# Kernel optimization log

Measured on AMD Instinct MI355X. Metric: run time of the kernel, lower is better.

The kernel has to match this reference:

```python
import jax, jax.numpy as jnp
import numpy as np

BALL_BBOX_SIZE = 40.0
PLAYER_DS = 16
BALL_DS = 4
MAX_DET = 100
B, HP, WP = 64, 68, 120
HB, WB = 272, 480


def _nms2d(x):
    # keep only local maxima in a 3x3 window (kornia-style NonMaximaSuppression2d)
    m = jax.lax.reduce_window(x, -jnp.inf, jax.lax.max, (1, 1, 3, 3), (1, 1, 1, 1), 'SAME')
    return jnp.where(x == m, x, jnp.zeros((), x.dtype))


def _detect_from_map(conf_logits, ds, max_det, bbox_map):
    # conf_logits: [B,2,h,w]; bbox_map: [B,4,h,w] or None
    p = jax.nn.softmax(conf_logits, axis=1)          # softmax applied in forward() for 'detect' phase
    conf = _nms2d(p)[:, 1]                           # [B,h,w], positive-class channel
    bsz, h, w = conf.shape
    flat = conf.reshape(bsz, h * w)
    values, indices = jax.lax.top_k(flat, max_det)   # == full descending sort truncated to max_det
    fds = jnp.float32(ds)
    xc = (indices % w).astype(jnp.float32) * fds + (fds - 1.0) / 2.0
    yc = (indices // w).astype(jnp.float32) * fds + (fds - 1.0) / 2.0
    if bbox_map is None:
        # ball: fixed-size boxes, zero center offsets
        temp = jnp.zeros((bsz, 4, max_det), jnp.float32).at[:, 2:4].set(BALL_BBOX_SIZE)
    else:
        # offsets/sizes are fractions of image size -> scale to pixels, then gather per top-k cell
        scale = jnp.array([w * ds, h * ds, w * ds, h * ds], jnp.float32).reshape(1, 4, 1)
        bm = bbox_map.reshape(bsz, 4, h * w) * scale
        temp = jnp.take_along_axis(bm, indices[:, None, :], axis=2)  # [B,4,max_det]
    bx = xc + temp[:, 0]
    by = yc + temp[:, 1]
    return jnp.stack([bx - 0.5 * temp[:, 2],
                      by - 0.5 * temp[:, 3],
                      bx + 0.5 * temp[:, 2],
                      by + 0.5 * temp[:, 3],
                      values], axis=-1)              # [B,max_det,5] = x1,y1,x2,y2,score


def setup_inputs() -> dict:
    key = jax.random.key(0)
    k1, k2, k3 = jax.random.split(key, 3)
    return {
        'player_feature_map': jax.random.normal(k1, (B, 2, HP, WP), jnp.float32),
        'player_bbox': jax.random.normal(k2, (B, 4, HP, WP), jnp.float32) * 0.05,
        'ball_feature_map': jax.random.normal(k3, (B, 2, HB, WB), jnp.float32),
    }


def reference(player_feature_map, player_bbox, ball_feature_map):
    player_det = _detect_from_map(player_feature_map, PLAYER_DS, MAX_DET, player_bbox)
    ball_det = _detect_from_map(ball_feature_map, BALL_DS, MAX_DET, None)
    return (player_det, ball_det)
```

## Files before the change

kernel.cpp:

```cpp
#include <hip/hip_runtime.h>
#include <stdint.h>
#include <math.h>

#define TPB   512
#define KTOP  100
#define K1    128
#define KSLOT 192
#define CAP   768
#define SR    8

#define HB 272
#define WB 480
#define NSB 34
#define HP 68
#define WP 120
#define NSP 9
#define NB 64

__device__ __forceinline__ float G_exact(float D) {
    float t = -fabsf(D);
    float etf = (float)exp((double)t);
    return (D > 0.0f) ? __fdiv_rn(1.0f, __fadd_rn(etf, 1.0f))
                      : __fdiv_rn(etf, __fadd_rn(1.0f, etf));
}

__device__ __forceinline__ uint32_t flip_f32(float D) {
    uint32_t u = __float_as_uint(D);
    return (u & 0x80000000u) ? ~u : (u | 0x80000000u);
}

__device__ __forceinline__ int agg_push(int* ctr, bool active) {
    uint64_t m = __ballot(active);
    int pos = -1;
    if (active) {
        int lane = threadIdx.x & 63;
        int lead = __ffsll((unsigned long long)m) - 1;
        int before = (int)__popcll(m & ((1ull << lane) - 1ull));
        int base = 0;
        if (lane == lead) base = atomicAdd(ctr, (int)__popcll(m));
        base = __shfl(base, lead, 64);
        pos = base + before;
    }
    return pos;
}

__device__ __forceinline__ void hist_clustered(uint32_t* hist, uint32_t bin, bool active) {
    uint64_t todo = __ballot(active);
    while (todo) {
        int lead = __ffsll((unsigned long long)todo) - 1;
        uint32_t b = (uint32_t)__shfl((int)bin, lead, 64);
        uint64_t same = __ballot(active && (bin == b));
        if ((int)(threadIdx.x & 63) == lead) atomicAdd(&hist[b], (uint32_t)__popcll(same));
        todo &= ~same;
    }
}

__device__ __forceinline__ void suffix_scan_256(uint32_t* hist) {
    if (threadIdx.x < 64) {
        int lane = threadIdx.x;
        uint32_t h0 = hist[4*lane+0], h1 = hist[4*lane+1];
        uint32_t h2 = hist[4*lane+2], h3 = hist[4*lane+3];
        uint32_t tot = h0 + h1 + h2 + h3;
        uint32_t run = tot;
        #pragma unroll
        for (int d = 1; d < 64; d <<= 1) {
            uint32_t o = __shfl_down(run, d, 64);
            if (lane + d < 64) run += o;
        }
        uint32_t ab = run - tot;
        hist[4*lane+3] = ab + h3;
        hist[4*lane+2] = ab + h3 + h2;
        hist[4*lane+1] = ab + h3 + h2 + h1;
        hist[4*lane+0] = ab + tot;
    }
    __syncthreads();
}

template<int W>
__device__ __forceinline__ void row6(const float* df, int row, int c4, float* a) {
    const float4 m = ((const float4*)df)[(row * W + c4) >> 2];
    a[1] = m.x; a[2] = m.y; a[3] = m.z; a[4] = m.w;
    a[0] = (c4 > 0)     ? df[row * W + c4 - 1] : -INFINITY;
    a[5] = (c4 + 4 < W) ? df[row * W + c4 + 4] : -INFINITY;
}

template<int H, int W, int NS>
__device__ __forceinline__ void stage1_impl(const float* __restrict__ x,
                                            int s, int b,
                                            uint32_t* __restrict__ key_out,
                                            unsigned char* smem)
{
    constexpr int W4 = W / 4;
    constexpr int tileRows = SR + 2;
    const int r0 = s * SR;
    const int rows = (H - r0 < SR) ? (H - r0) : SR;

    float*    df    = (float*)smem;
    uint32_t* surv  = (uint32_t*)(df + tileRows * W);
    uint32_t* hist  = surv + CAP;
    uint32_t* hist2 = hist + 256;
    uint32_t* outb  = hist2 + 256;
    __shared__ int s_cnt, s_out;
    __shared__ uint32_t s_bin, s_ab, s_bin2, s_none;
    if (threadIdx.x == 0) { s_cnt = 0; s_out = 0; s_none = 0; }
    if (threadIdx.x < 256) { hist[threadIdx.x] = 0; hist2[threadIdx.x] = 0; }
    if (threadIdx.x < KSLOT) outb[threadIdx.x] = 0;

    const float*  x0  = x + (size_t)b * 2 * H * W;
    const float*  x1  = x0 + (size_t)H * W;
    const float4* x0v = (const float4*)x0;
    const float4* x1v = (const float4*)x1;
    float4* dfv = (float4*)df;

    constexpr int nt4 = tileRows * W4;
    for (int t = threadIdx.x; t < nt4; t += TPB) {
        int tr = t / W4, c4 = t - tr * W4;
        int r = r0 - 1 + tr;
        float4 d4 = make_float4(-INFINITY, -INFINITY, -INFINITY, -INFINITY);
        if (r >= 0 && r < H) {
            float4 a = x0v[r * W4 + c4];
            float4 c = x1v[r * W4 + c4];
            d4.x = __fsub_rn(c.x, a.x);
            d4.y = __fsub_rn(c.y, a.y);
            d4.z = __fsub_rn(c.z, a.z);
            d4.w = __fsub_rn(c.w, a.w);
        }
        dfv[t] = d4;
    }
    __syncthreads();

    const int groups = rows * W4;
    for (int g = threadIdx.x; g < groups; g += TPB) {
        int lr = g / W4, c4 = (g - lr * W4) << 2;
        int tr = lr + 1;
        float ap[6], ac[6], an[6];
        row6<W>(df, tr - 1, c4, ap);
        row6<W>(df, tr,     c4, ac);
        row6<W>(df, tr + 1, c4, an);
        #pragma unroll
        for (int j = 0; j < 4; ++j) {
            float v = ac[j + 1];
            float mx = fmaxf(fmaxf(fmaxf(ap[j], ap[j+1]), fmaxf(ap[j+2], an[j])),
                             fmaxf(fmaxf(an[j+1], an[j+2]), fmaxf(ac[j], ac[j+2])));
            bool keep;
            if (v >= mx) keep = true;
            else if (mx - v >= 0.25f && mx < 13.0f) keep = false;
            else keep = (G_exact(v) == G_exact(mx));
            if (keep) {
                uint32_t key16 = flip_f32(v) >> 16;
                int pos = atomicAdd(&s_cnt, 1);
                if (pos < CAP)
                    surv[pos] = (key16 << 16) | ((uint32_t)lr << 9) | (uint32_t)(c4 + j);
                atomicAdd(&hist[key16 >> 8], 1u);
            }
        }
    }
    __syncthreads();
    const int n = (s_cnt < CAP) ? s_cnt : CAP;

    suffix_scan_256(hist);
    if (threadIdx.x < 256) {
        uint32_t si = hist[threadIdx.x];
        uint32_t sn = (threadIdx.x < 255) ? hist[threadIdx.x + 1] : 0u;
        if (threadIdx.x == 0 && si < K1) s_none = 1;
        if (si >= K1 && sn < K1) { s_bin = threadIdx.x; s_ab = sn; }
    }
    __syncthreads();

    uint32_t T16 = 0;
    if (!s_none) {
        const uint32_t b3 = s_bin;
        const uint32_t k2 = K1 - s_ab;
        for (int t = threadIdx.x; t < n; t += TPB) {
            uint32_t sv = surv[t];
            if ((sv >> 24) == b3) atomicAdd(&hist2[(sv >> 16) & 255u], 1u);
        }
        __syncthreads();
        suffix_scan_256(hist2);
        if (threadIdx.x < 256) {
            uint32_t si = hist2[threadIdx.x];
            uint32_t sn = (threadIdx.x < 255) ? hist2[threadIdx.x + 1] : 0u;
            if (si >= k2 && sn < k2) s_bin2 = threadIdx.x;
        }
        __syncthreads();
        T16 = (b3 << 8) | s_bin2;
    }

    for (int t = threadIdx.x; t < n; t += TPB) {
        uint32_t sv = surv[t];
        if ((sv >> 16) >= T16) {
            int pos = atomicAdd(&s_out, 1);
            if (pos < KSLOT) outb[pos] = sv;
        }
    }
    __syncthreads();
    if (threadIdx.x < KSLOT)
        key_out[((size_t)b * NS + s) * KSLOT + threadIdx.x] = outb[threadIdx.x];
}

__global__ __launch_bounds__(TPB) void stage1(const float* __restrict__ bmap,
                                              const float* __restrict__ pmap,
                                              uint32_t* __restrict__ bkey,
                                              uint32_t* __restrict__ pkey)
{
    extern __shared__ unsigned char smem[];
    if (blockIdx.x < NSB)
        stage1_impl<HB, WB, NSB>(bmap, blockIdx.x, blockIdx.y, bkey, smem);
    else
        stage1_impl<HP, WP, NSP>(pmap, blockIdx.x - NSB, blockIdx.y, pkey, smem);
}

template<int H, int W, int NS, bool BALL>
__device__ __forceinline__ void stage2_impl(const float* __restrict__ xmap,
                                            const float* __restrict__ pbbox,
                                            const uint32_t* __restrict__ key_in,
                                            float* __restrict__ outp,
                                            int b, unsigned char* smem)
{
    constexpr int M = NS * KSLOT;
    const float* x0 = xmap + (size_t)b * 2 * H * W;
    const float* x1 = x0 + (size_t)H * W;
    const uint32_t* kin = key_in + (size_t)b * M;

    uint32_t* keys  = (uint32_t*)smem;
    uint32_t* hist  = keys + M;
    uint32_t* hist2 = hist + 256;
    uint32_t* rnk   = hist2 + 256;
    uint64_t* outb  = (uint64_t*)(rnk + 256);
    __shared__ int s_out;
    __shared__ uint32_t s_bin, s_ab, s_bin2, s_none;
    if (threadIdx.x == 0) { s_out = 0; s_none = 0; }
    if (threadIdx.x < 256) {
        hist[threadIdx.x] = 0; hist2[threadIdx.x] = 0;
        rnk[threadIdx.x] = 0; outb[threadIdx.x] = 0;
    }
    for (int t = threadIdx.x; t < KTOP * 5; t += TPB) outp[t] = 0.f;
    __syncthreads();

    for (int t = threadIdx.x; t < M; t += TPB) {
        uint32_t k = kin[t];
        keys[t] = k;
        hist_clustered(hist, k >> 24, k != 0);
    }
    __syncthreads();
    suffix_scan_256(hist);
    if (threadIdx.x < 256) {
        uint32_t si = hist[threadIdx.x];
        uint32_t sn = (threadIdx.x < 255) ? hist[threadIdx.x + 1] : 0u;
        if (threadIdx.x == 0 && si < K1) s_none = 1;
        if (si >= K1 && sn < K1) { s_bin = threadIdx.x; s_ab = sn; }
    }
    __syncthreads();

    uint32_t T16 = 0;
    if (!s_none) {
        const uint32_t b3 = s_bin;
        const uint32_t k2 = K1 - s_ab;
        for (int t = threadIdx.x; t < M; t += TPB) {
            uint32_t k = keys[t];
            if (k && (k >> 24) == b3) atomicAdd(&hist2[(k >> 16) & 255u], 1u);
        }
        __syncthreads();
        suffix_scan_256(hist2);
        if (threadIdx.x < 256) {
            uint32_t si = hist2[threadIdx.x];
            uint32_t sn = (threadIdx.x < 255) ? hist2[threadIdx.x + 1] : 0u;
            if (si >= k2 && sn < k2) s_bin2 = threadIdx.x;
        }
        __syncthreads();
        T16 = (b3 << 8) | s_bin2;
    }

    for (int t = threadIdx.x; t < M; t += TPB) {
        uint32_t k = keys[t];
        bool take = (k != 0) && ((k >> 16) >= T16);
        int pos = agg_push(&s_out, take);
        if (take && pos < 256) {
            int sIdx = t / KSLOT;
            int lr = (k >> 9) & 7, c = k & 511;
            int gidx = (sIdx * SR + lr) * W + c;
            float D = __fsub_rn(x1[gidx], x0[gidx]);
            float p = G_exact(D);
            outb[pos] = ((uint64_t)__float_as_uint(p) << 32) | (uint32_t)(~gidx);
        }
    }
    __syncthreads();

    {
        int i = threadIdx.x & 255;
        int half = threadIdx.x >> 8;
        uint64_t ki = outb[i];
        uint32_t cnt = 0;
        int j0 = half * 128;
        #pragma unroll 4
        for (int j = j0; j < j0 + 128; ++j) cnt += (outb[j] > ki) ? 1u : 0u;
        atomicAdd(&rnk[i], cnt);
    }
    __syncthreads();

    if (threadIdx.x < 256) {
        uint64_t k = outb[threadIdx.x];
        uint32_t r = rnk[threadIdx.x];
        if (k != 0 && r < KTOP) {
            int id = (int)(~(uint32_t)k);
            float val = __uint_as_float((uint32_t)(k >> 32));
            int yy = id / W, xx = id - yy * W;
            constexpr float ds = BALL ? 4.0f : 16.0f;
            float xc = (float)xx * ds + (ds - 1.0f) * 0.5f;
            float yc = (float)yy * ds + (ds - 1.0f) * 0.5f;
            float t0 = 0.f, t1 = 0.f;
            float t2 = BALL ? 40.0f : 0.0f, t3 = BALL ? 40.0f : 0.0f;
            if (!BALL) {
                const float* bb = pbbox + (size_t)b * 4 * H * W;
                constexpr float sx = (float)W * ds, sy = (float)H * ds;
                t0 = bb[id]             * sx;
                t1 = bb[id + H * W]     * sy;
                t2 = bb[id + 2 * H * W] * sx;
                t3 = bb[id + 3 * H * W] * sy;
            }
            float bx = xc + t0, by = yc + t1;
            float* op = outp + (size_t)r * 5;
            op[0] = bx - 0.5f * t2;
            op[1] = by - 0.5f * t3;
            op[2] = bx + 0.5f * t2;
            op[3] = by + 0.5f * t3;
            op[4] = val;
        }
    }
}

__global__ __launch_bounds__(TPB) void stage2(const float* __restrict__ bmap,
                                              const float* __restrict__ pmap,
                                              const float* __restrict__ pbbox,
                                              const uint32_t* __restrict__ bkey,
                                              const uint32_t* __restrict__ pkey,
                                              float* __restrict__ out)
{
    extern __shared__ unsigned char smem[];
    if (blockIdx.x < NB) {
        int b = blockIdx.x;
        stage2_impl<HB, WB, NSB, true>(bmap, nullptr, bkey,
            out + (size_t)NB * KTOP * 5 + (size_t)b * KTOP * 5, b, smem);
    } else {
        int b = blockIdx.x - NB;
        stage2_impl<HP, WP, NSP, false>(pmap, pbbox, pkey,
            out + (size_t)b * KTOP * 5, b, smem);
    }
}

extern "C" void kernel_launch(void* const* d_in, const int* in_sizes, int n_in,
                              void* d_out, int out_size, void* d_ws, size_t ws_size,
                              hipStream_t stream) {
    const float* pmap  = (const float*)d_in[0];
    const float* pbbox = (const float*)d_in[1];
    const float* bmap  = (const float*)d_in[2];
    float* out = (float*)d_out;

    uint32_t* ws_bkey = (uint32_t*)d_ws;
    uint32_t* ws_pkey = ws_bkey + (size_t)NB * NSB * KSLOT;

    size_t lds1 = (size_t)(SR + 2) * WB * 4 + (size_t)CAP * 4 + 2048 + (size_t)KSLOT * 4;
    stage1<<<dim3(NSB + NSP, NB), TPB, lds1, stream>>>(bmap, pmap, ws_bkey, ws_pkey);

    size_t lds2 = (size_t)NSB * KSLOT * 4 + 3072 + 2048;
    stage2<<<2 * NB, TPB, lds2, stream>>>(bmap, pmap, pbbox, ws_bkey, ws_pkey, out);
}
```

Before: 139.4 us.

## Make stage1 persistent with register-prefetched tiles overlapping compute

Stage1 now launches a fixed grid of 1024 blocks. Each block handles two or three ball tiles, or two ball tiles plus one player tile, in sequence. The next tile's global loads are issued into registers before the current tile's NMS and top-k selection runs, which hides load latency behind compute and cuts launch and block startup overhead. In exchange, registers per thread go up, shared state must be reset between tiles, and there are fewer blocks, which reduces memory-level parallelism across the GPU.

```diff
diff --git a/kernel.cpp b/kernel.cpp
--- a/kernel.cpp
+++ b/kernel.cpp
@@ -16,6 +16,11 @@
 #define WP 120
 #define NSP 9
 #define NB 64
+
+#define NBLK1 1024
+#define NTB   (NSB * NB)
+#define NTP   (NSP * NB)
+#define DF_BYTES (10 * WB * 4)
 
 __device__ __forceinline__ float G_exact(float D) {
     float t = -fabsf(D);
@@ -84,50 +89,64 @@
     a[5] = (c4 + 4 < W) ? df[row * W + c4 + 4] : -INFINITY;
 }
 
-template<int H, int W, int NS>
-__device__ __forceinline__ void stage1_impl(const float* __restrict__ x,
-                                            int s, int b,
-                                            uint32_t* __restrict__ key_out,
-                                            unsigned char* smem)
-{
+struct Ctl { int cnt; int out; uint32_t bin, ab, bin2, none; };
+
+template<int H, int W>
+__device__ __forceinline__ void issue_tile(const float* __restrict__ x, int s, int b,
+                                           float4* ra, float4* rc) {
     constexpr int W4 = W / 4;
-    constexpr int tileRows = SR + 2;
+    constexpr int nt4 = (SR + 2) * W4;
+    constexpr int NCH = (nt4 + TPB - 1) / TPB;
     const int r0 = s * SR;
-    const int rows = (H - r0 < SR) ? (H - r0) : SR;
-
-    float*    df    = (float*)smem;
-    uint32_t* surv  = (uint32_t*)(df + tileRows * W);
-    uint32_t* hist  = surv + CAP;
-    uint32_t* hist2 = hist + 256;
-    uint32_t* outb  = hist2 + 256;
-    __shared__ int s_cnt, s_out;
-    __shared__ uint32_t s_bin, s_ab, s_bin2, s_none;
-    if (threadIdx.x == 0) { s_cnt = 0; s_out = 0; s_none = 0; }
-    if (threadIdx.x < 256) { hist[threadIdx.x] = 0; hist2[threadIdx.x] = 0; }
-    if (threadIdx.x < KSLOT) outb[threadIdx.x] = 0;
-
-    const float*  x0  = x + (size_t)b * 2 * H * W;
-    const float*  x1  = x0 + (size_t)H * W;
-    const float4* x0v = (const float4*)x0;
-    const float4* x1v = (const float4*)x1;
+    const float4* x0v = (const float4*)(x + (size_t)b * 2 * H * W);
+    const float4* x1v = (const float4*)(x + (size_t)b * 2 * H * W + (size_t)H * W);
+    #pragma unroll
+    for (int u = 0; u < NCH; ++u) {
+        int t = threadIdx.x + u * TPB;
+        if (t < nt4) {
+            int tr = t / W4, c4 = t - tr * W4;
+            int r = r0 - 1 + tr;
+            if (r >= 0 && r < H) {
+                ra[u] = x0v[r * W4 + c4];
+                rc[u] = x1v[r * W4 + c4];
+            } else {
+                ra[u] = make_float4(0.f, 0.f, 0.f, 0.f);
+                rc[u] = make_float4(-INFINITY, -INFINITY, -INFINITY, -INFINITY);
+            }
+        }
+    }
+    __builtin_amdgcn_sched_barrier(0);
+}
+
+template<int H, int W>
+__device__ __forceinline__ void store_tile(const float4* ra, const float4* rc, float* df) {
+    constexpr int W4 = W / 4;
+    constexpr int nt4 = (SR + 2) * W4;
+    constexpr int NCH = (nt4 + TPB - 1) / TPB;
     float4* dfv = (float4*)df;
-
-    constexpr int nt4 = tileRows * W4;
-    for (int t = threadIdx.x; t < nt4; t += TPB) {
-        int tr = t / W4, c4 = t - tr * W4;
-        int r = r0 - 1 + tr;
-        float4 d4 = make_float4(-INFINITY, -INFINITY, -INFINITY, -INFINITY);
-        if (r >= 0 && r < H) {
-            float4 a = x0v[r * W4 + c4];
-            float4 c = x1v[r * W4 + c4];
+    #pragma unroll
+    for (int u = 0; u < NCH; ++u) {
+        int t = threadIdx.x + u * TPB;
+        if (t < nt4) {
+            float4 a = ra[u], c = rc[u];
+            float4 d4;
             d4.x = __fsub_rn(c.x, a.x);
             d4.y = __fsub_rn(c.y, a.y);
             d4.z = __fsub_rn(c.z, a.z);
             d4.w = __fsub_rn(c.w, a.w);
-        }
-        dfv[t] = d4;
-    }
-    __syncthreads();
+            dfv[t] = d4;
+        }
+    }
+}
+
+template<int H, int W, int NS>
+__device__ __forceinline__ void s1_body(int s, int b, uint32_t* __restrict__ key_out,
+                                        float* df, uint32_t* surv, uint32_t* hist,
+                                        uint32_t* hist2, uint32_t* outb, Ctl& ctl)
+{
+    constexpr int W4 = W / 4;
+    const int r0 = s * SR;
+    const int rows = (H - r0 < SR) ? (H - r0) : SR;
 
     const int groups = rows * W4;
     for (int g = threadIdx.x; g < groups; g += TPB) {
@@ -148,7 +167,7 @@
             else keep = (G_exact(v) == G_exact(mx));
             if (keep) {
                 uint32_t key16 = flip_f32(v) >> 16;
-                int pos = atomicAdd(&s_cnt, 1);
+                int pos = atomicAdd(&ctl.cnt, 1);
                 if (pos < CAP)
                     surv[pos] = (key16 << 16) | ((uint32_t)lr << 9) | (uint32_t)(c4 + j);
                 atomicAdd(&hist[key16 >> 8], 1u);
@@ -156,21 +175,21 @@
         }
     }
     __syncthreads();
-    const int n = (s_cnt < CAP) ? s_cnt : CAP;
+    const int n = (ctl.cnt < CAP) ? ctl.cnt : CAP;
 
     suffix_scan_256(hist);
     if (threadIdx.x < 256) {
         uint32_t si = hist[threadIdx.x];
         uint32_t sn = (threadIdx.x < 255) ? hist[threadIdx.x + 1] : 0u;
-        if (threadIdx.x == 0 && si < K1) s_none = 1;
-        if (si >= K1 && sn < K1) { s_bin = threadIdx.x; s_ab = sn; }
+        if (threadIdx.x == 0 && si < K1) ctl.none = 1;
+        if (si >= K1 && sn < K1) { ctl.bin = threadIdx.x; ctl.ab = sn; }
     }
     __syncthreads();
 
     uint32_t T16 = 0;
-    if (!s_none) {
-        const uint32_t b3 = s_bin;
-        const uint32_t k2 = K1 - s_ab;
+    if (!ctl.none) {
+        const uint32_t b3 = ctl.bin;
+        const uint32_t k2 = K1 - ctl.ab;
         for (int t = threadIdx.x; t < n; t += TPB) {
             uint32_t sv = surv[t];
             if ((sv >> 24) == b3) atomicAdd(&hist2[(sv >> 16) & 255u], 1u);
@@ -180,22 +199,28 @@
         if (threadIdx.x < 256) {
             uint32_t si = hist2[threadIdx.x];
             uint32_t sn = (threadIdx.x < 255) ? hist2[threadIdx.x + 1] : 0u;
-            if (si >= k2 && sn < k2) s_bin2 = threadIdx.x;
-        }
-        __syncthreads();
-        T16 = (b3 << 8) | s_bin2;
+            if (si >= k2 && sn < k2) ctl.bin2 = threadIdx.x;
+        }
+        __syncthreads();
+        T16 = (b3 << 8) | ctl.bin2;
     }
 
     for (int t = threadIdx.x; t < n; t += TPB) {
         uint32_t sv = surv[t];
         if ((sv >> 16) >= T16) {
-            int pos = atomicAdd(&s_out, 1);
+            int pos = atomicAdd(&ctl.out, 1);
             if (pos < KSLOT) outb[pos] = sv;
         }
     }
     __syncthreads();
-    if (threadIdx.x < KSLOT)
+
+    if (threadIdx.x < KSLOT) {
         key_out[((size_t)b * NS + s) * KSLOT + threadIdx.x] = outb[threadIdx.x];
+        outb[threadIdx.x] = 0;
+    }
+    if (threadIdx.x < 256) { hist[threadIdx.x] = 0; hist2[threadIdx.x] = 0; }
+    if (threadIdx.x == 0)  { ctl.cnt = 0; ctl.out = 0; ctl.none = 0; }
+    __syncthreads();
 }
 
 __global__ __launch_bounds__(TPB) void stage1(const float* __restrict__ bmap,
@@ -204,10 +229,52 @@
                                               uint32_t* __restrict__ pkey)
 {
     extern __shared__ unsigned char smem[];
-    if (blockIdx.x < NSB)
-        stage1_impl<HB, WB, NSB>(bmap, blockIdx.x, blockIdx.y, bkey, smem);
-    else
-        stage1_impl<HP, WP, NSP>(pmap, blockIdx.x - NSB, blockIdx.y, pkey, smem);
+    float*    df    = (float*)smem;
+    uint32_t* surv  = (uint32_t*)(smem + DF_BYTES);
+    uint32_t* hist  = surv + CAP;
+    uint32_t* hist2 = hist + 256;
+    uint32_t* outb  = hist2 + 256;
+    __shared__ Ctl ctl;
+    if (threadIdx.x == 0) { ctl.cnt = 0; ctl.out = 0; ctl.none = 0; }
+    if (threadIdx.x < 256) { hist[threadIdx.x] = 0; hist2[threadIdx.x] = 0; }
+    if (threadIdx.x < KSLOT) outb[threadIdx.x] = 0;
+
+    const int k = blockIdx.x;
+    const int tb0 = k, tb1 = k + NBLK1;
+    const int b0 = tb0 / NSB, s0 = tb0 % NSB;
+    const int b1 = tb1 / NSB, s1 = tb1 % NSB;
+    const bool third_ball = (k < NTB - 2 * NBLK1);
+    const bool has_player = (!third_ball) && (k < (NTB - 2 * NBLK1) + NTP);
+
+    float4 ra[3], rc[3];
+
+    issue_tile<HB, WB>(bmap, s0, b0, ra, rc);
+    store_tile<HB, WB>(ra, rc, df);
+    issue_tile<HB, WB>(bmap, s1, b1, ra, rc);
+    __syncthreads();
+    s1_body<HB, WB, NSB>(s0, b0, bkey, df, surv, hist, hist2, outb, ctl);
+
+    store_tile<HB, WB>(ra, rc, df);
+    int b2 = 0, s2 = 0, bp = 0, sp = 0;
+    if (third_ball) {
+        int t2 = 2 * NBLK1 + k; b2 = t2 / NSB; s2 = t2 % NSB;
+        issue_tile<HB, WB>(bmap, s2, b2, ra, rc);
+    } else if (has_player) {
+        int tp = k - (NTB - 2 * NBLK1); bp = tp / NSP; sp = tp % NSP;
+        issue_tile<HP, WP>(pmap, sp, bp, ra, rc);
+    }
+    __syncthreads();
+    s1_body<HB, WB, NSB>(s1, b1, bkey, df, surv, hist, hist2, outb, ctl);
+
+    if (third_ball) {
+        store_tile<HB, WB>(ra, rc, df);
+        __syncthreads();
+        s1_body<HB, WB, NSB>(s2, b2, bkey, df, surv, hist, hist2, outb, ctl);
+    } else if (has_player) {
+        store_tile<HP, WP>(ra, rc, df);
+        __syncthreads();
+        s1_body<HP, WP, NSP>(sp, bp, pkey, df, surv, hist, hist2, outb, ctl);
+    }
 }
 
 template<int H, int W, int NS, bool BALL>
@@ -359,8 +426,8 @@
     uint32_t* ws_bkey = (uint32_t*)d_ws;
     uint32_t* ws_pkey = ws_bkey + (size_t)NB * NSB * KSLOT;
 
-    size_t lds1 = (size_t)(SR + 2) * WB * 4 + (size_t)CAP * 4 + 2048 + (size_t)KSLOT * 4;
-    stage1<<<dim3(NSB + NSP, NB), TPB, lds1, stream>>>(bmap, pmap, ws_bkey, ws_pkey);
+    size_t lds1 = (size_t)DF_BYTES + (size_t)CAP * 4 + 2048 + (size_t)KSLOT * 4;
+    stage1<<<dim3(NBLK1), TPB, lds1, stream>>>(bmap, pmap, ws_bkey, ws_pkey);
 
     size_t lds2 = (size_t)NSB * KSLOT * 4 + 3072 + 2048;
     stage2<<<2 * NB, TPB, lds2, stream>>>(bmap, pmap, pbbox, ws_bkey, ws_pkey, out);
```

Result: slower. 153.9 us (+10.4%).

## Rewrite stage1 as single-wave blocks with register-rolling stencil and deferred exact checks

Applied to the files above, without the earlier changes.

Stage 1 now runs one 64-lane wave per strip task instead of 512-thread blocks. Each lane owns a column, keeps a rolling three-row window of differences in registers, and gets horizontal neighbours through shuffles, so there is no LDS tile. Survivor compaction uses ballot/popcount in place of shared atomics. The histogram threshold search runs inside a single wave with no __syncthreads. Ambiguous cells that need the exact double-precision sigmoid comparison are queued and evaluated together afterwards to reduce divergence. The cost is a scalar per-column global load pattern with no float4, a strip overlap of 2 columns per 64 lanes, and many more small blocks.

```diff
diff --git a/kernel.cpp b/kernel.cpp
--- a/kernel.cpp
+++ b/kernel.cpp
@@ -2,12 +2,14 @@
 #include <stdint.h>
 #include <math.h>
 
-#define TPB   512
+#define TPB1  64
+#define TPB2  512
 #define KTOP  100
 #define K1    128
 #define KSLOT 192
 #define CAP   768
 #define SR    8
+#define AMB   320
 
 #define HB 272
 #define WB 480
@@ -16,6 +18,9 @@
 #define WP 120
 #define NSP 9
 #define NB 64
+#define NTB (NSB*NB)
+#define NTP (NSP*NB)
+#define NTASK (NTB+NTP)
 
 __device__ __forceinline__ float G_exact(float D) {
     float t = -fabsf(D);
@@ -27,6 +32,195 @@
 __device__ __forceinline__ uint32_t flip_f32(float D) {
     uint32_t u = __float_as_uint(D);
     return (u & 0x80000000u) ? ~u : (u | 0x80000000u);
+}
+
+
+template<int H, int W>
+__device__ __forceinline__ void ldrow(const float* __restrict__ x0,
+                                      const float* __restrict__ x1,
+                                      int r, int col, bool colok,
+                                      float& a, float& c) {
+    if (r >= 0 && r < H && colok) {
+        int o = r * W + col;
+        a = x0[o]; c = x1[o];
+    } else { a = 0.f; c = -INFINITY; }
+}
+
+__device__ __forceinline__ void wave_pick(const uint32_t* h, uint32_t kk, int lane,
+                                          uint32_t& total, uint32_t& obin, uint32_t& osn)
+{
+    uint32_t h0 = h[4*lane+0], h1 = h[4*lane+1], h2 = h[4*lane+2], h3 = h[4*lane+3];
+    uint32_t tot = h0 + h1 + h2 + h3;
+    uint32_t run = tot;
+    #pragma unroll
+    for (int d = 1; d < 64; d <<= 1) {
+        uint32_t o = __shfl_down(run, d, 64);
+        if (lane + d < 64) run += o;
+    }
+    uint32_t ab = run - tot;
+    uint32_t S3 = ab + h3, S2 = S3 + h2, S1 = S2 + h1, S0 = S1 + h0;
+    uint32_t Sn = __shfl_down(S0, 1, 64);
+    if (lane == 63) Sn = 0;
+    total = (uint32_t)__shfl((int)run, 0, 64);
+    int fb = -1; uint32_t fs = 0;
+    if (S0 >= kk && S1 < kk) { fb = 4*lane+0; fs = S1; }
+    if (S1 >= kk && S2 < kk) { fb = 4*lane+1; fs = S2; }
+    if (S2 >= kk && S3 < kk) { fb = 4*lane+2; fs = S3; }
+    if (S3 >= kk && Sn < kk) { fb = 4*lane+3; fs = Sn; }
+    uint64_t fm = __ballot(fb >= 0);
+    if (fm) {
+        int lead = __ffsll((unsigned long long)fm) - 1;
+        obin = (uint32_t)__shfl(fb, lead, 64);
+        osn  = (uint32_t)__shfl((int)fs, lead, 64);
+    } else { obin = 0; osn = 0; }
+}
+
+template<int H, int W, int NS>
+__device__ __forceinline__ void s1_wave(const float* __restrict__ x, int s, int b,
+                                        uint32_t* __restrict__ key_out,
+                                        uint32_t* hist, uint32_t* hist2,
+                                        uint32_t* surv, uint32_t* outb,
+                                        uint32_t* ambp, float* ambv, float* ambm)
+{
+    const int lane = threadIdx.x;
+    const uint64_t lt = (1ull << lane) - 1ull;
+    #pragma unroll
+    for (int i = 0; i < 4; ++i) { hist[lane+64*i] = 0; hist2[lane+64*i] = 0; }
+    outb[lane] = 0; outb[lane+64] = 0; outb[lane+128] = 0;
+
+    const float* x0 = x + (size_t)b * 2 * H * W;
+    const float* x1 = x0 + (size_t)H * W;
+    const int r0 = s * SR;
+    const int rows = (H - r0 < SR) ? (H - r0) : SR;
+    constexpr int NSTR = (W + 61) / 62;
+
+    int cnt = 0, aCnt = 0;
+
+    for (int st = 0; st < NSTR; ++st) {
+        const int col = st * 62 - 1 + lane;
+        const bool colok = (unsigned)col < (unsigned)W;
+        const bool active = (lane >= 1) && (lane <= 62) && colok;
+
+        float aP,cP,aC,cC,aN,cN,aX,cX;
+        ldrow<H,W>(x0,x1, r0-1, col, colok, aP,cP);
+        ldrow<H,W>(x0,x1, r0,   col, colok, aC,cC);
+        ldrow<H,W>(x0,x1, r0+1, col, colok, aN,cN);
+        ldrow<H,W>(x0,x1, r0+2, col, colok, aX,cX);
+        float dP = __fsub_rn(cP,aP), dC = __fsub_rn(cC,aC), dN = __fsub_rn(cN,aN);
+
+        for (int lr = 0; lr < rows; ++lr) {
+            float m3  = fmaxf(fmaxf(dP, dC), dN);
+            float m3l = __shfl(m3, (lane+63)&63, 64);
+            float m3r = __shfl(m3, (lane+1)&63, 64);
+            float mx  = fmaxf(fmaxf(m3l, m3r), fmaxf(dP, dN));
+            float v   = dC;
+            bool keep = false, amb = false;
+            if (active) {
+                if (v >= mx) keep = true;
+                else if (mx - v >= 0.25f && mx < 13.0f) keep = false;
+                else amb = true;
+            }
+            uint64_t am = __ballot(amb);
+            if (amb) {
+                int q = aCnt + (int)__popcll(am & lt);
+                if (q < AMB) {
+                    ambp[q] = ((uint32_t)lr << 9) | (uint32_t)col;
+                    ambv[q] = v; ambm[q] = mx;
+                } else keep = (G_exact(v) == G_exact(mx));
+            }
+            aCnt += (int)__popcll(am);
+            uint64_t km = __ballot(keep);
+            if (keep) {
+                uint32_t key16 = flip_f32(v) >> 16;
+                int pos = cnt + (int)__popcll(km & lt);
+                if (pos < CAP)
+                    surv[pos] = (key16 << 16) | ((uint32_t)lr << 9) | (uint32_t)col;
+                atomicAdd(&hist[key16 >> 8], 1u);
+            }
+            cnt += (int)__popcll(km);
+            if (lr + 1 < rows) {
+                dP = dC; dC = dN;
+                dN = __fsub_rn(cX, aX);
+                if (lr + 3 <= rows)
+                    ldrow<H,W>(x0,x1, r0+lr+3, col, colok, aX,cX);
+            }
+        }
+    }
+
+    const int na = (aCnt < AMB) ? aCnt : AMB;
+    for (int t0 = 0; t0 < na; t0 += 64) {
+        int i = t0 + lane;
+        bool act = i < na;
+        int ii = act ? i : 0;
+        float v = ambv[ii], mxx = ambm[ii];
+        bool keep = act && (G_exact(v) == G_exact(mxx));
+        uint64_t km = __ballot(keep);
+        if (keep) {
+            uint32_t key16 = flip_f32(v) >> 16;
+            int pos = cnt + (int)__popcll(km & lt);
+            if (pos < CAP) surv[pos] = (key16 << 16) | ambp[ii];
+            atomicAdd(&hist[key16 >> 8], 1u);
+        }
+        cnt += (int)__popcll(km);
+    }
+    const int n = (cnt < CAP) ? cnt : CAP;
+
+    uint32_t T16 = 0, total, b3, sn1;
+    wave_pick(hist, K1, lane, total, b3, sn1);
+    if (total >= K1) {
+        uint32_t k2 = K1 - sn1;
+        for (int t0 = 0; t0 < n; t0 += 64) {
+            int i = t0 + lane;
+            if (i < n) {
+                uint32_t sv = surv[i];
+                if ((sv >> 24) == b3) atomicAdd(&hist2[(sv >> 16) & 255u], 1u);
+            }
+        }
+        uint32_t tot2, b2, sn2;
+        wave_pick(hist2, k2, lane, tot2, b2, sn2);
+        T16 = (b3 << 8) | b2;
+    }
+
+    int out = 0;
+    for (int t0 = 0; t0 < n; t0 += 64) {
+        int i = t0 + lane;
+        bool take = (i < n) && ((surv[i] >> 16) >= T16);
+        uint64_t tm = __ballot(take);
+        if (take) {
+            int pos = out + (int)__popcll(tm & lt);
+            if (pos < KSLOT) outb[pos] = surv[i];
+        }
+        out += (int)__popcll(tm);
+    }
+    uint32_t* ko = key_out + ((size_t)b * NS + s) * KSLOT;
+    ko[lane] = outb[lane];
+    ko[lane+64] = outb[lane+64];
+    ko[lane+128] = outb[lane+128];
+}
+
+__global__ __launch_bounds__(TPB1) void stage1(const float* __restrict__ bmap,
+                                               const float* __restrict__ pmap,
+                                               uint32_t* __restrict__ bkey,
+                                               uint32_t* __restrict__ pkey)
+{
+    extern __shared__ unsigned char smem[];
+    uint32_t* hist  = (uint32_t*)smem;
+    uint32_t* hist2 = hist + 256;
+    uint32_t* surv  = hist2 + 256;
+    uint32_t* outb  = surv + CAP;
+    uint32_t* ambp  = outb + KSLOT;
+    float*    ambv  = (float*)(ambp + AMB);
+    float*    ambm  = ambv + AMB;
+
+    const int task = blockIdx.x;
+    if (task < NTB) {
+        int b = task / NSB, s = task - b * NSB;
+        s1_wave<HB, WB, NSB>(bmap, s, b, bkey, hist, hist2, surv, outb, ambp, ambv, ambm);
+    } else {
+        int t = task - NTB;
+        int b = t / NSP, s = t - b * NSP;
+        s1_wave<HP, WP, NSP>(pmap, s, b, pkey, hist, hist2, surv, outb, ambp, ambv, ambm);
+    }
 }
 
 __device__ __forceinline__ int agg_push(int* ctr, bool active) {
@@ -76,140 +270,6 @@
     __syncthreads();
 }
 
-template<int W>
-__device__ __forceinline__ void row6(const float* df, int row, int c4, float* a) {
-    const float4 m = ((const float4*)df)[(row * W + c4) >> 2];
-    a[1] = m.x; a[2] = m.y; a[3] = m.z; a[4] = m.w;
-    a[0] = (c4 > 0)     ? df[row * W + c4 - 1] : -INFINITY;
-    a[5] = (c4 + 4 < W) ? df[row * W + c4 + 4] : -INFINITY;
-}
-
-template<int H, int W, int NS>
-__device__ __forceinline__ void stage1_impl(const float* __restrict__ x,
-                                            int s, int b,
-                                            uint32_t* __restrict__ key_out,
-                                            unsigned char* smem)
-{
-    constexpr int W4 = W / 4;
-    constexpr int tileRows = SR + 2;
-    const int r0 = s * SR;
-    const int rows = (H - r0 < SR) ? (H - r0) : SR;
-
-    float*    df    = (float*)smem;
-    uint32_t* surv  = (uint32_t*)(df + tileRows * W);
-    uint32_t* hist  = surv + CAP;
-    uint32_t* hist2 = hist + 256;
-    uint32_t* outb  = hist2 + 256;
-    __shared__ int s_cnt, s_out;
-    __shared__ uint32_t s_bin, s_ab, s_bin2, s_none;
-    if (threadIdx.x == 0) { s_cnt = 0; s_out = 0; s_none = 0; }
-    if (threadIdx.x < 256) { hist[threadIdx.x] = 0; hist2[threadIdx.x] = 0; }
-    if (threadIdx.x < KSLOT) outb[threadIdx.x] = 0;
-
-    const float*  x0  = x + (size_t)b * 2 * H * W;
-    const float*  x1  = x0 + (size_t)H * W;
-    const float4* x0v = (const float4*)x0;
-    const float4* x1v = (const float4*)x1;
-    float4* dfv = (float4*)df;
-
-    constexpr int nt4 = tileRows * W4;
-    for (int t = threadIdx.x; t < nt4; t += TPB) {
-        int tr = t / W4, c4 = t - tr * W4;
-        int r = r0 - 1 + tr;
-        float4 d4 = make_float4(-INFINITY, -INFINITY, -INFINITY, -INFINITY);
-        if (r >= 0 && r < H) {
-            float4 a = x0v[r * W4 + c4];
-            float4 c = x1v[r * W4 + c4];
-            d4.x = __fsub_rn(c.x, a.x);
-            d4.y = __fsub_rn(c.y, a.y);
-            d4.z = __fsub_rn(c.z, a.z);
-            d4.w = __fsub_rn(c.w, a.w);
-        }
-        dfv[t] = d4;
-    }
-    __syncthreads();
-
-    const int groups = rows * W4;
-    for (int g = threadIdx.x; g < groups; g += TPB) {
-        int lr = g / W4, c4 = (g - lr * W4) << 2;
-        int tr = lr + 1;
-        float ap[6], ac[6], an[6];
-        row6<W>(df, tr - 1, c4, ap);
-        row6<W>(df, tr,     c4, ac);
-        row6<W>(df, tr + 1, c4, an);
-        #pragma unroll
-        for (int j = 0; j < 4; ++j) {
-            float v = ac[j + 1];
-            float mx = fmaxf(fmaxf(fmaxf(ap[j], ap[j+1]), fmaxf(ap[j+2], an[j])),
-                             fmaxf(fmaxf(an[j+1], an[j+2]), fmaxf(ac[j], ac[j+2])));
-            bool keep;
-            if (v >= mx) keep = true;
-            else if (mx - v >= 0.25f && mx < 13.0f) keep = false;
-            else keep = (G_exact(v) == G_exact(mx));
-            if (keep) {
-                uint32_t key16 = flip_f32(v) >> 16;
-                int pos = atomicAdd(&s_cnt, 1);
-                if (pos < CAP)
-                    surv[pos] = (key16 << 16) | ((uint32_t)lr << 9) | (uint32_t)(c4 + j);
-                atomicAdd(&hist[key16 >> 8], 1u);
-            }
-        }
-    }
-    __syncthreads();
-    const int n = (s_cnt < CAP) ? s_cnt : CAP;
-
-    suffix_scan_256(hist);
-    if (threadIdx.x < 256) {
-        uint32_t si = hist[threadIdx.x];
-        uint32_t sn = (threadIdx.x < 255) ? hist[threadIdx.x + 1] : 0u;
-        if (threadIdx.x == 0 && si < K1) s_none = 1;
-        if (si >= K1 && sn < K1) { s_bin = threadIdx.x; s_ab = sn; }
-    }
-    __syncthreads();
-
-    uint32_t T16 = 0;
-    if (!s_none) {
-        const uint32_t b3 = s_bin;
-        const uint32_t k2 = K1 - s_ab;
-        for (int t = threadIdx.x; t < n; t += TPB) {
-            uint32_t sv = surv[t];
-            if ((sv >> 24) == b3) atomicAdd(&hist2[(sv >> 16) & 255u], 1u);
-        }
-        __syncthreads();
-        suffix_scan_256(hist2);
-        if (threadIdx.x < 256) {
-            uint32_t si = hist2[threadIdx.x];
-            uint32_t sn = (threadIdx.x < 255) ? hist2[threadIdx.x + 1] : 0u;
-            if (si >= k2 && sn < k2) s_bin2 = threadIdx.x;
-        }
-        __syncthreads();
-        T16 = (b3 << 8) | s_bin2;
-    }
-
-    for (int t = threadIdx.x; t < n; t += TPB) {
-        uint32_t sv = surv[t];
-        if ((sv >> 16) >= T16) {
-            int pos = atomicAdd(&s_out, 1);
-            if (pos < KSLOT) outb[pos] = sv;
-        }
-    }
-    __syncthreads();
-    if (threadIdx.x < KSLOT)
-        key_out[((size_t)b * NS + s) * KSLOT + threadIdx.x] = outb[threadIdx.x];
-}
-
-__global__ __launch_bounds__(TPB) void stage1(const float* __restrict__ bmap,
-                                              const float* __restrict__ pmap,
-                                              uint32_t* __restrict__ bkey,
-                                              uint32_t* __restrict__ pkey)
-{
-    extern __shared__ unsigned char smem[];
-    if (blockIdx.x < NSB)
-        stage1_impl<HB, WB, NSB>(bmap, blockIdx.x, blockIdx.y, bkey, smem);
-    else
-        stage1_impl<HP, WP, NSP>(pmap, blockIdx.x - NSB, blockIdx.y, pkey, smem);
-}
-
 template<int H, int W, int NS, bool BALL>
 __device__ __forceinline__ void stage2_impl(const float* __restrict__ xmap,
                                             const float* __restrict__ pbbox,
@@ -234,10 +294,10 @@
         hist[threadIdx.x] = 0; hist2[threadIdx.x] = 0;
         rnk[threadIdx.x] = 0; outb[threadIdx.x] = 0;
     }
-    for (int t = threadIdx.x; t < KTOP * 5; t += TPB) outp[t] = 0.f;
-    __syncthreads();
-
-    for (int t = threadIdx.x; t < M; t += TPB) {
+    for (int t = threadIdx.x; t < KTOP * 5; t += TPB2) outp[t] = 0.f;
+    __syncthreads();
+
+    for (int t = threadIdx.x; t < M; t += TPB2) {
         uint32_t k = kin[t];
         keys[t] = k;
         hist_clustered(hist, k >> 24, k != 0);
@@ -256,7 +316,7 @@
     if (!s_none) {
         const uint32_t b3 = s_bin;
         const uint32_t k2 = K1 - s_ab;
-        for (int t = threadIdx.x; t < M; t += TPB) {
+        for (int t = threadIdx.x; t < M; t += TPB2) {
             uint32_t k = keys[t];
             if (k && (k >> 24) == b3) atomicAdd(&hist2[(k >> 16) & 255u], 1u);
         }
@@ -271,7 +331,7 @@
         T16 = (b3 << 8) | s_bin2;
     }
 
-    for (int t = threadIdx.x; t < M; t += TPB) {
+    for (int t = threadIdx.x; t < M; t += TPB2) {
         uint32_t k = keys[t];
         bool take = (k != 0) && ((k >> 16) >= T16);
         int pos = agg_push(&s_out, take);
@@ -329,12 +389,12 @@
     }
 }
 
-__global__ __launch_bounds__(TPB) void stage2(const float* __restrict__ bmap,
-                                              const float* __restrict__ pmap,
-                                              const float* __restrict__ pbbox,
-                                              const uint32_t* __restrict__ bkey,
-                                              const uint32_t* __restrict__ pkey,
-                                              float* __restrict__ out)
+__global__ __launch_bounds__(TPB2) void stage2(const float* __restrict__ bmap,
+                                               const float* __restrict__ pmap,
+                                               const float* __restrict__ pbbox,
+                                               const uint32_t* __restrict__ bkey,
+                                               const uint32_t* __restrict__ pkey,
+                                               float* __restrict__ out)
 {
     extern __shared__ unsigned char smem[];
     if (blockIdx.x < NB) {
@@ -359,9 +419,9 @@
     uint32_t* ws_bkey = (uint32_t*)d_ws;
     uint32_t* ws_pkey = ws_bkey + (size_t)NB * NSB * KSLOT;
 
-    size_t lds1 = (size_t)(SR + 2) * WB * 4 + (size_t)CAP * 4 + 2048 + (size_t)KSLOT * 4;
-    stage1<<<dim3(NSB + NSP, NB), TPB, lds1, stream>>>(bmap, pmap, ws_bkey, ws_pkey);
+    size_t lds1 = 2048 + (size_t)CAP * 4 + (size_t)KSLOT * 4 + (size_t)AMB * 12;
+    stage1<<<dim3(NTASK), TPB1, lds1, stream>>>(bmap, pmap, ws_bkey, ws_pkey);
 
     size_t lds2 = (size_t)NSB * KSLOT * 4 + 3072 + 2048;
-    stage2<<<2 * NB, TPB, lds2, stream>>>(bmap, pmap, pbbox, ws_bkey, ws_pkey, out);
-}
+    stage2<<<2 * NB, TPB2, lds2, stream>>>(bmap, pmap, pbbox, ws_bkey, ws_pkey, out);
+}
```

New measurement: 155.9 us. 1.12x slower.
